# Kernel optimization log

Measured on AMD Instinct MI355X. Metric: run time of the kernel, lower is better.

The kernel has to match this reference:

```python
import jax, jax.numpy as jnp
import numpy as np

B, T, D, M = 8, 4096, 64, 1024  # batch, frames, embedding_dim, codebook size


def setup_inputs() -> dict:
    key = jax.random.key(0)
    k1, k2, k3 = jax.random.split(key, 3)
    x = jax.random.normal(k1, (B, D, T), dtype=jnp.float32)          # (B, channels=D, T)
    embedding = jax.random.normal(k2, (M, D), dtype=jnp.float32)     # codebook
    # Precomputed Gumbel noise, matching torch: -log(-log(clamp(U, eps, 1-eps)))
    eps = jnp.finfo(jnp.float32).eps
    u = jax.random.uniform(k3, (B * T, M), dtype=jnp.float32)
    gumbels = -jnp.log(-jnp.log(jnp.clip(u, eps, 1.0 - eps)))
    log_var_q = jnp.float32(0.0)
    temperature = jnp.float32(0.5)
    return {"x": x, "embedding": embedding, "log_var_q": log_var_q,
            "gumbels": gumbels, "temperature": temperature}


def reference(x, embedding, log_var_q, gumbels, temperature):
    B_, D_, T_ = x.shape
    M_ = embedding.shape[0]
    xt = jnp.swapaxes(x, 1, 2)                 # (B, T, D)
    x_flat = xt.reshape(-1, D_)                # (N, D)
    precision = jnp.exp(-log_var_q)            # scalar
    # 0.5 * precision * ||x - e||^2, via the GEMM expansion (fused cdist)
    sq = (jnp.sum(x_flat * x_flat, axis=1, keepdims=True)
          + jnp.sum(embedding * embedding, axis=1)[None, :]
          - 2.0 * x_flat @ embedding.T)        # (N, M)
    distances = 0.5 * precision * sq
    indices = jnp.argmin(distances, axis=-1)   # (N,)
    logits = -distances
    # gumbel-softmax (soft)
    encodings = jax.nn.softmax((logits + gumbels) / temperature, axis=-1)  # (N, M)
    quantized = (encodings @ embedding).reshape(B_, T_, D_)                # (B, T, D)
    logits3 = logits.reshape(B_, T_, M_)
    log_probs = jax.nn.log_softmax(logits3, axis=-1)
    probs = jnp.exp(log_probs)
    recon = 0.5 * precision * jnp.sum((xt - quantized) ** 2, axis=(1, 2))  # (B,)
    neg_entropy = jnp.sum(probs * log_probs, axis=(1, 2))                  # (B,)
    loss = jnp.mean(recon + neg_entropy)
    # perplexity over hard assignments
    one_hot = jax.nn.one_hot(indices, M_, dtype=jnp.float32)               # (N, M)
    avg_probs = jnp.mean(one_hot, axis=0)
    perplexity = jnp.exp(-jnp.sum(avg_probs * jnp.log(avg_probs + 1e-10)))
    return jnp.swapaxes(quantized, 1, 2), loss, perplexity
```

## Files before the change

kernel.cpp:

```cpp
#include <hip/hip_runtime.h>

#define T_DIM 4096
#define D_DIM 64
#define M_DIM 1024
#define N_ROWS 32768
#define TR 16
#define NT 512
#define NW 8

typedef __attribute__((ext_vector_type(8))) short bf16x8;
typedef __attribute__((ext_vector_type(4))) float f32x4;

#define WS_BF16_OFF 4096

__device__ __forceinline__ short f2bfs(float f) {
  union { float f; unsigned u; } v; v.f = f;
  unsigned r = v.u + 0x7fffu + ((v.u >> 16) & 1u);
  return (short)(r >> 16);
}
__device__ __forceinline__ float bf2f(short h) {
  union { unsigned u; float f; } v; v.u = ((unsigned)(unsigned short)h) << 16;
  return v.f;
}
__device__ __forceinline__ void cvt8(const float* p, bf16x8& h8, bf16x8& l8) {
  float4 a = *(const float4*)p, b = *(const float4*)(p + 4);
  float v[8] = {a.x, a.y, a.z, a.w, b.x, b.y, b.z, b.w};
#pragma unroll
  for (int i = 0; i < 8; ++i) {
    short h = f2bfs(v[i]);
    h8[i] = h;
    l8[i] = f2bfs(v[i] - bf2f(h));
  }
}

__global__ void vq_conv(const float* __restrict__ emb, float* __restrict__ ws) {
  __shared__ short s_h[64][72], s_l[64][72];
  const int tid = threadIdx.x;
  const int mb = blockIdx.x * 64;
  short* EH = (short*)(ws + WS_BF16_OFF);
  short* EL = EH + 65536;
  short* ETH = EL + 65536;
  short* ETL = ETH + 65536;
#pragma unroll
  for (int i = 0; i < 16; ++i) {
    int lin = tid + 256 * i;
    int ml = lin >> 6, d = lin & 63;
    float v = emb[(size_t)(mb + ml) * 64 + d];
    short h = f2bfs(v);
    short l = f2bfs(v - bf2f(h));
    EH[(size_t)(mb + ml) * 64 + d] = h;
    EL[(size_t)(mb + ml) * 64 + d] = l;
    s_h[d][ml] = h;
    s_l[d][ml] = l;
  }
  if (tid < 64) {
    const float* e = emb + (size_t)(mb + tid) * 64;
    float s = 0.f;
#pragma unroll
    for (int d = 0; d < 64; d += 4) {
      float4 v = *(const float4*)(e + d);
      s += v.x * v.x + v.y * v.y + v.z * v.z + v.w * v.w;
    }
    ws[mb + tid] = s;
    ws[M_DIM + mb + tid] = 0.f;
  }
  if (blockIdx.x == 0 && tid == 0) ws[2 * M_DIM] = 0.f;
  __syncthreads();
#pragma unroll
  for (int i = 0; i < 16; ++i) {
    int lin = tid + 256 * i;
    int d = lin >> 6, ml = lin & 63;
    ETH[(size_t)d * 1024 + mb + ml] = s_h[d][ml];
    ETL[(size_t)d * 1024 + mb + ml] = s_l[d][ml];
  }
}

__global__ __launch_bounds__(NT, 4) void vq_main(
    const float* __restrict__ x, const float* __restrict__ emb,
    const float* __restrict__ lvq, const float* __restrict__ gum,
    const float* __restrict__ temp, float* __restrict__ outq,
    float* __restrict__ ws) {
  __shared__ float s_x[TR][68];
  __shared__ float s_xx[TR];
  __shared__ float s_qp[NW][TR][68];
  __shared__ float s_stA_m[NW][TR];
  __shared__ int   s_stA_i[NW][TR];
  __shared__ float s_stB[NW][TR][3];
  __shared__ float s_stC[NW][TR];
  __shared__ float s_red[NW];

  const int tid = threadIdx.x;
  const int lane = tid & 63;
  const int wl = tid >> 6;
  const int mq = lane >> 4;
  const int mn = lane & 15;
  const int n0 = blockIdx.x * TR;
  const int b = n0 >> 12;
  const int t0 = n0 & (T_DIM - 1);
  const float precision = __expf(-lvq[0]);
  const float inv_temp = 1.0f / temp[0];
  const float* eew = ws;
  float* counts = ws + M_DIM;
  float* accum = ws + 2 * M_DIM;
  const short* EH = (const short*)(ws + WS_BF16_OFF);
  const short* EL = EH + 65536;
  const short* ETH = EL + 65536;
  const short* ETL = ETH + 65536;

  {
    int tt = tid & 15, d0 = tid >> 4;
    s_x[tt][d0] = x[((size_t)b << 18) + ((size_t)d0 << 12) + (size_t)(t0 + tt)];
    s_x[tt][d0 + 32] =
        x[((size_t)b << 18) + ((size_t)(d0 + 32) << 12) + (size_t)(t0 + tt)];
  }
  __syncthreads();
  if (tid < TR) {
    float s = 0.f;
#pragma unroll
    for (int d = 0; d < D_DIM; ++d) { float v = s_x[tid][d]; s += v * v; }
    s_xx[tid] = s;
  }
  __syncthreads();

  f32x4 acc[8];
  {
    bf16x8 ah0, al0, ah1, al1;
    cvt8(&s_x[mn][mq * 8], ah0, al0);
    cvt8(&s_x[mn][32 + mq * 8], ah1, al1);
#pragma unroll
    for (int tt = 0; tt < 8; ++tt) acc[tt] = (f32x4){0.f, 0.f, 0.f, 0.f};
#pragma unroll
    for (int tt = 0; tt < 8; ++tt) {
      int m0 = wl * 128 + tt * 16;
      const short* bp = EH + (m0 + mn) * 64 + mq * 8;
      const short* lp = EL + (m0 + mn) * 64 + mq * 8;
      bf16x8 bh0 = *(const bf16x8*)bp;
      bf16x8 bh1 = *(const bf16x8*)(bp + 32);
      bf16x8 bl0 = *(const bf16x8*)lp;
      bf16x8 bl1 = *(const bf16x8*)(lp + 32);
      acc[tt] = __builtin_amdgcn_mfma_f32_16x16x32_bf16(ah0, bh0, acc[tt], 0, 0, 0);
      acc[tt] = __builtin_amdgcn_mfma_f32_16x16x32_bf16(ah1, bh1, acc[tt], 0, 0, 0);
      acc[tt] = __builtin_amdgcn_mfma_f32_16x16x32_bf16(al0, bh0, acc[tt], 0, 0, 0);
      acc[tt] = __builtin_amdgcn_mfma_f32_16x16x32_bf16(al1, bh1, acc[tt], 0, 0, 0);
      acc[tt] = __builtin_amdgcn_mfma_f32_16x16x32_bf16(ah0, bl0, acc[tt], 0, 0, 0);
      acc[tt] = __builtin_amdgcn_mfma_f32_16x16x32_bf16(ah1, bl1, acc[tt], 0, 0, 0);
    }
    float xx4[4];
#pragma unroll
    for (int reg = 0; reg < 4; ++reg) xx4[reg] = s_xx[mq * 4 + reg];
#pragma unroll
    for (int tt = 0; tt < 8; ++tt) {
      float eev = eew[wl * 128 + tt * 16 + mn];
#pragma unroll
      for (int reg = 0; reg < 4; ++reg)
        acc[tt][reg] = precision * (acc[tt][reg] - 0.5f * (xx4[reg] + eev));
    }
  }

  float Mx[4]; int Mi[4];
#pragma unroll
  for (int reg = 0; reg < 4; ++reg) {
    float mx = acc[0][reg]; int mi = wl * 128 + mn;
#pragma unroll
    for (int tt = 1; tt < 8; ++tt) {
      float v = acc[tt][reg];
      int m = wl * 128 + tt * 16 + mn;
      if (v > mx) { mx = v; mi = m; }
    }
#pragma unroll
    for (int off = 1; off <= 8; off <<= 1) {
      float omx = __shfl_xor(mx, off);
      int omi = __shfl_xor(mi, off);
      if (omx > mx || (omx == mx && omi < mi)) { mx = omx; mi = omi; }
    }
    if (mn == 0) { s_stA_m[wl][mq * 4 + reg] = mx; s_stA_i[wl][mq * 4 + reg] = mi; }
  }
  __syncthreads();
#pragma unroll
  for (int reg = 0; reg < 4; ++reg) {
    int token = mq * 4 + reg;
    Mx[reg] = s_stA_m[0][token]; Mi[reg] = s_stA_i[0][token];
#pragma unroll
    for (int w = 1; w < NW; ++w) {
      float m2 = s_stA_m[w][token]; int i2 = s_stA_i[w][token];
      if (m2 > Mx[reg] || (m2 == Mx[reg] && i2 < Mi[reg])) { Mx[reg] = m2; Mi[reg] = i2; }
    }
  }
  float partial = 0.f;
  if (wl == 0 && mn == 0) {
#pragma unroll
    for (int reg = 0; reg < 4; ++reg) atomicAdd(counts + Mi[reg], 1.0f);
  }

  float Zs[4] = {0.f, 0.f, 0.f, 0.f}, As[4] = {0.f, 0.f, 0.f, 0.f}, Gm[4];
#pragma unroll
  for (int reg = 0; reg < 4; ++reg) {
    const float* gp = gum + ((size_t)(n0 + mq * 4 + reg) << 10) + wl * 128 + mn;
    float gm = -1e30f;
#pragma unroll
    for (int tt = 0; tt < 8; ++tt) {
      float g = gp[tt * 16];
      float s = acc[tt][reg];
      float a = s - Mx[reg];
      float e = __expf(a);
      Zs[reg] += e; As[reg] += a * e;
      float gv = (s + g) * inv_temp;
      acc[tt][reg] = gv;
      gm = fmaxf(gm, gv);
    }
    Gm[reg] = gm;
  }
#pragma unroll
  for (int reg = 0; reg < 4; ++reg) {
#pragma unroll
    for (int off = 1; off <= 8; off <<= 1) {
      Zs[reg] += __shfl_xor(Zs[reg], off);
      As[reg] += __shfl_xor(As[reg], off);
      Gm[reg] = fmaxf(Gm[reg], __shfl_xor(Gm[reg], off));
    }
    if (mn == 0) {
      s_stB[wl][mq * 4 + reg][0] = Zs[reg];
      s_stB[wl][mq * 4 + reg][1] = As[reg];
      s_stB[wl][mq * 4 + reg][2] = Gm[reg];
    }
  }
  __syncthreads();
  float GM[4];
#pragma unroll
  for (int reg = 0; reg < 4; ++reg) {
    int token = mq * 4 + reg;
    float zs = 0.f, as = 0.f, gmax = -1e30f;
#pragma unroll
    for (int w = 0; w < NW; ++w) {
      zs += s_stB[w][token][0];
      as += s_stB[w][token][1];
      gmax = fmaxf(gmax, s_stB[w][token][2]);
    }
    GM[reg] = gmax;
    if (wl == 0 && mn == 0) partial += as / zs - __logf(zs);
  }
  float Zg[4] = {0.f, 0.f, 0.f, 0.f};
#pragma unroll
  for (int tt = 0; tt < 8; ++tt) {
#pragma unroll
    for (int reg = 0; reg < 4; ++reg) {
      float p = __expf(acc[tt][reg] - GM[reg]);
      acc[tt][reg] = p;
      Zg[reg] += p;
    }
  }
#pragma unroll
  for (int reg = 0; reg < 4; ++reg) {
#pragma unroll
    for (int off = 1; off <= 8; off <<= 1) Zg[reg] += __shfl_xor(Zg[reg], off);
    if (mn == 0) s_stC[wl][mq * 4 + reg] = Zg[reg];
  }
  __syncthreads();
  float invZg[4];
#pragma unroll
  for (int reg = 0; reg < 4; ++reg) {
    int token = mq * 4 + reg;
    float z = 0.f;
#pragma unroll
    for (int w = 0; w < NW; ++w) z += s_stC[w][token];
    invZg[reg] = 1.0f / z;
  }

  {
    f32x4 q[4];
#pragma unroll
    for (int nt = 0; nt < 4; ++nt) q[nt] = (f32x4){0.f, 0.f, 0.f, 0.f};
    float* sp = &s_qp[wl][0][0];
#pragma unroll
    for (int ks = 0; ks < 4; ++ks) {
#pragma unroll
      for (int reg = 0; reg < 4; ++reg) {
        sp[(mq * 4 + reg) * 36 + mn]      = acc[2 * ks][reg] * invZg[reg];
        sp[(mq * 4 + reg) * 36 + 16 + mn] = acc[2 * ks + 1][reg] * invZg[reg];
      }
      bf16x8 ph, pl;
      cvt8(&sp[mn * 36 + mq * 8], ph, pl);
      int k0 = wl * 128 + ks * 32;
#pragma unroll
      for (int nt = 0; nt < 4; ++nt) {
        const short* bp = ETH + (nt * 16 + mn) * 1024 + k0 + mq * 8;
        const short* lp = ETL + (nt * 16 + mn) * 1024 + k0 + mq * 8;
        bf16x8 bh = *(const bf16x8*)bp;
        bf16x8 bl = *(const bf16x8*)lp;
        q[nt] = __builtin_amdgcn_mfma_f32_16x16x32_bf16(ph, bh, q[nt], 0, 0, 0);
        q[nt] = __builtin_amdgcn_mfma_f32_16x16x32_bf16(pl, bh, q[nt], 0, 0, 0);
        q[nt] = __builtin_amdgcn_mfma_f32_16x16x32_bf16(ph, bl, q[nt], 0, 0, 0);
      }
    }
#pragma unroll
    for (int nt = 0; nt < 4; ++nt)
#pragma unroll
      for (int reg = 0; reg < 4; ++reg)
        s_qp[wl][mq * 4 + reg][nt * 16 + mn] = q[nt][reg];
  }
  __syncthreads();

  if (tid < 256) {
    int r = tid & 15, dq = tid >> 4;
    float4 qs = {0.f, 0.f, 0.f, 0.f};
#pragma unroll
    for (int w = 0; w < NW; ++w) {
      float4 v = *(const float4*)&s_qp[w][r][4 * dq];
      qs.x += v.x; qs.y += v.y; qs.z += v.z; qs.w += v.w;
    }
    int t = t0 + r;
    float* ob = outq + ((size_t)b << 18) + (size_t)t;
    int d = 4 * dq;
    ob[(size_t)(d + 0) << 12] = qs.x;
    ob[(size_t)(d + 1) << 12] = qs.y;
    ob[(size_t)(d + 2) << 12] = qs.z;
    ob[(size_t)(d + 3) << 12] = qs.w;
    float4 xv = *(const float4*)&s_x[r][d];
    float dx0 = xv.x - qs.x, dx1 = xv.y - qs.y, dx2 = xv.z - qs.z, dx3 = xv.w - qs.w;
    partial += 0.5f * precision * (dx0 * dx0 + dx1 * dx1 + dx2 * dx2 + dx3 * dx3);
  }
#pragma unroll
  for (int off = 32; off; off >>= 1) partial += __shfl_xor(partial, off);
  if (lane == 0) s_red[wl] = partial;
  __syncthreads();
  if (tid == 0) {
    float s = 0.f;
#pragma unroll
    for (int w = 0; w < NW; ++w) s += s_red[w];
    atomicAdd(accum, s);
  }
}

__global__ void vq_finalize(const float* __restrict__ ws, float* __restrict__ out) {
  __shared__ float red[4];
  int tid = threadIdx.x;
  float h = 0.f;
  for (int m = tid; m < M_DIM; m += 256) {
    float avg = ws[M_DIM + m] * (1.0f / 32768.0f);
    h += avg * __logf(avg + 1e-10f);
  }
#pragma unroll
  for (int off = 32; off; off >>= 1) h += __shfl_xor(h, off);
  int lane = tid & 63, wave = tid >> 6;
  if (lane == 0) red[wave] = h;
  __syncthreads();
  if (tid == 0) {
    out[0] = ws[2 * M_DIM] * 0.125f;
    out[1] = __expf(-(red[0] + red[1] + red[2] + red[3]));
  }
}

extern "C" void kernel_launch(void* const* d_in, const int* in_sizes, int n_in,
                              void* d_out, int out_size, void* d_ws, size_t ws_size,
                              hipStream_t stream) {
  const float* x = (const float*)d_in[0];
  const float* emb = (const float*)d_in[1];
  const float* lvq = (const float*)d_in[2];
  const float* gum = (const float*)d_in[3];
  const float* temp = (const float*)d_in[4];
  float* out = (float*)d_out;
  float* ws = (float*)d_ws;

  hipLaunchKernelGGL(vq_conv, dim3(16), dim3(256), 0, stream, emb, ws);
  hipLaunchKernelGGL(vq_main, dim3(N_ROWS / TR), dim3(NT), 0, stream,
                     x, emb, lvq, gum, temp, out, ws);
  hipLaunchKernelGGL(vq_finalize, dim3(1), dim3(256), 0, stream, ws,
                     out + (size_t)2097152);
}
```

Before: 316.8 us.

## Prefetch gumbel noise before GEMM and merge softmax reduction barriers

Gumbel noise values are loaded into registers before the distance MFMA, so their global-memory latency overlaps the matrix work instead of stalling the softmax pass. The per-wave Gumbel max is used locally and rescaled afterward in an online-softmax style, which merges the stats into one float4 and removes a __syncthreads plus a shared-memory round. The final reduction also spreads across all 512 threads with float2 work. The prefetch adds 32 live registers per thread, which risks occupancy under launch_bounds(512,4).

```diff
diff --git a/kernel.cpp b/kernel.cpp
--- a/kernel.cpp
+++ b/kernel.cpp
@@ -83,10 +83,8 @@
   __shared__ float s_x[TR][68];
   __shared__ float s_xx[TR];
   __shared__ float s_qp[NW][TR][68];
-  __shared__ float s_stA_m[NW][TR];
-  __shared__ int   s_stA_i[NW][TR];
-  __shared__ float s_stB[NW][TR][3];
-  __shared__ float s_stC[NW][TR];
+  __shared__ float2 s_stA[NW][TR];
+  __shared__ float4 s_stB[NW][TR];
   __shared__ float s_red[NW];
 
   const int tid = threadIdx.x;
@@ -122,6 +120,18 @@
   }
   __syncthreads();
 
+  float gpre[8][4];
+  {
+    const float* gp0 = gum + ((size_t)(n0 + mq * 4) << 10) + (size_t)(wl * 128 + mn);
+#pragma unroll
+    for (int reg = 0; reg < 4; ++reg) {
+#pragma unroll
+      for (int tt = 0; tt < 8; ++tt)
+        gpre[tt][reg] = gp0[((size_t)reg << 10) + tt * 16];
+    }
+  }
+  __builtin_amdgcn_sched_barrier(0);
+
   f32x4 acc[8];
   {
     bf16x8 ah0, al0, ah1, al1;
@@ -173,18 +183,21 @@
       int omi = __shfl_xor(mi, off);
       if (omx > mx || (omx == mx && omi < mi)) { mx = omx; mi = omi; }
     }
-    if (mn == 0) { s_stA_m[wl][mq * 4 + reg] = mx; s_stA_i[wl][mq * 4 + reg] = mi; }
+    if (mn == 0) s_stA[wl][mq * 4 + reg] = make_float2(mx, __int_as_float(mi));
   }
   __syncthreads();
 #pragma unroll
   for (int reg = 0; reg < 4; ++reg) {
     int token = mq * 4 + reg;
-    Mx[reg] = s_stA_m[0][token]; Mi[reg] = s_stA_i[0][token];
+    float2 a0 = s_stA[0][token];
+    float mx = a0.x; int mi = __float_as_int(a0.y);
 #pragma unroll
     for (int w = 1; w < NW; ++w) {
-      float m2 = s_stA_m[w][token]; int i2 = s_stA_i[w][token];
-      if (m2 > Mx[reg] || (m2 == Mx[reg] && i2 < Mi[reg])) { Mx[reg] = m2; Mi[reg] = i2; }
-    }
+      float2 aw = s_stA[w][token];
+      int i2 = __float_as_int(aw.y);
+      if (aw.x > mx || (aw.x == mx && i2 < mi)) { mx = aw.x; mi = i2; }
+    }
+    Mx[reg] = mx; Mi[reg] = mi;
   }
   float partial = 0.f;
   if (wl == 0 && mn == 0) {
@@ -195,11 +208,10 @@
   float Zs[4] = {0.f, 0.f, 0.f, 0.f}, As[4] = {0.f, 0.f, 0.f, 0.f}, Gm[4];
 #pragma unroll
   for (int reg = 0; reg < 4; ++reg) {
-    const float* gp = gum + ((size_t)(n0 + mq * 4 + reg) << 10) + wl * 128 + mn;
     float gm = -1e30f;
 #pragma unroll
     for (int tt = 0; tt < 8; ++tt) {
-      float g = gp[tt * 16];
+      float g = gpre[tt][reg];
       float s = acc[tt][reg];
       float a = s - Mx[reg];
       float e = __expf(a);
@@ -218,33 +230,13 @@
       As[reg] += __shfl_xor(As[reg], off);
       Gm[reg] = fmaxf(Gm[reg], __shfl_xor(Gm[reg], off));
     }
-    if (mn == 0) {
-      s_stB[wl][mq * 4 + reg][0] = Zs[reg];
-      s_stB[wl][mq * 4 + reg][1] = As[reg];
-      s_stB[wl][mq * 4 + reg][2] = Gm[reg];
-    }
-  }
-  __syncthreads();
-  float GM[4];
-#pragma unroll
-  for (int reg = 0; reg < 4; ++reg) {
-    int token = mq * 4 + reg;
-    float zs = 0.f, as = 0.f, gmax = -1e30f;
-#pragma unroll
-    for (int w = 0; w < NW; ++w) {
-      zs += s_stB[w][token][0];
-      as += s_stB[w][token][1];
-      gmax = fmaxf(gmax, s_stB[w][token][2]);
-    }
-    GM[reg] = gmax;
-    if (wl == 0 && mn == 0) partial += as / zs - __logf(zs);
   }
   float Zg[4] = {0.f, 0.f, 0.f, 0.f};
 #pragma unroll
   for (int tt = 0; tt < 8; ++tt) {
 #pragma unroll
     for (int reg = 0; reg < 4; ++reg) {
-      float p = __expf(acc[tt][reg] - GM[reg]);
+      float p = __expf(acc[tt][reg] - Gm[reg]);
       acc[tt][reg] = p;
       Zg[reg] += p;
     }
@@ -253,17 +245,26 @@
   for (int reg = 0; reg < 4; ++reg) {
 #pragma unroll
     for (int off = 1; off <= 8; off <<= 1) Zg[reg] += __shfl_xor(Zg[reg], off);
-    if (mn == 0) s_stC[wl][mq * 4 + reg] = Zg[reg];
+    if (mn == 0)
+      s_stB[wl][mq * 4 + reg] = make_float4(Zs[reg], As[reg], Gm[reg], Zg[reg]);
   }
   __syncthreads();
   float invZg[4];
 #pragma unroll
   for (int reg = 0; reg < 4; ++reg) {
     int token = mq * 4 + reg;
-    float z = 0.f;
-#pragma unroll
-    for (int w = 0; w < NW; ++w) z += s_stC[w][token];
-    invZg[reg] = 1.0f / z;
+    float gmax = -1e30f;
+#pragma unroll
+    for (int w = 0; w < NW; ++w) gmax = fmaxf(gmax, s_stB[w][token].z);
+    float zs = 0.f, as = 0.f, zg = 0.f;
+#pragma unroll
+    for (int w = 0; w < NW; ++w) {
+      float4 v = s_stB[w][token];
+      zs += v.x; as += v.y;
+      zg += v.w * __expf(v.z - gmax);
+    }
+    invZg[reg] = __expf(Gm[reg] - gmax) / zg;
+    if (wl == 0 && mn == 0) partial += as / zs - __logf(zs);
   }
 
   {
@@ -300,24 +301,22 @@
   }
   __syncthreads();
 
-  if (tid < 256) {
+  {
     int r = tid & 15, dq = tid >> 4;
-    float4 qs = {0.f, 0.f, 0.f, 0.f};
+    int d = dq * 2;
+    float2 qs = {0.f, 0.f};
 #pragma unroll
     for (int w = 0; w < NW; ++w) {
-      float4 v = *(const float4*)&s_qp[w][r][4 * dq];
-      qs.x += v.x; qs.y += v.y; qs.z += v.z; qs.w += v.w;
+      float2 v = *(const float2*)&s_qp[w][r][d];
+      qs.x += v.x; qs.y += v.y;
     }
     int t = t0 + r;
     float* ob = outq + ((size_t)b << 18) + (size_t)t;
-    int d = 4 * dq;
     ob[(size_t)(d + 0) << 12] = qs.x;
     ob[(size_t)(d + 1) << 12] = qs.y;
-    ob[(size_t)(d + 2) << 12] = qs.z;
-    ob[(size_t)(d + 3) << 12] = qs.w;
-    float4 xv = *(const float4*)&s_x[r][d];
-    float dx0 = xv.x - qs.x, dx1 = xv.y - qs.y, dx2 = xv.z - qs.z, dx3 = xv.w - qs.w;
-    partial += 0.5f * precision * (dx0 * dx0 + dx1 * dx1 + dx2 * dx2 + dx3 * dx3);
+    float2 xv = *(const float2*)&s_x[r][d];
+    float dx0 = xv.x - qs.x, dx1 = xv.y - qs.y;
+    partial += 0.5f * precision * (dx0 * dx0 + dx1 * dx1);
   }
 #pragma unroll
   for (int off = 32; off; off >>= 1) partial += __shfl_xor(partial, off);
```

Result: slower. 325.1 us (+2.6%).
